# Optimization experiments

Measured on AMD Instinct MI355X. Metric: run time of the kernel, lower is better.

The kernel has to match this reference:

```python
import jax, jax.numpy as jnp
import numpy as np

C_IN = 2048
N_EXP = 64
TOPK = 2


def setup_inputs() -> dict:
    key = jax.random.key(0)
    kx, kw, kb = jax.random.split(key, 3)
    x = jax.random.normal(kx, (4, 4096, C_IN), dtype=jnp.float32)
    # nn.Linear(c_in, n_exp): weight [n_exp, c_in], bias [n_exp]
    bound = 1.0 / np.sqrt(C_IN)
    W = jax.random.uniform(kw, (N_EXP, C_IN), minval=-bound, maxval=bound, dtype=jnp.float32)
    b = jax.random.uniform(kb, (N_EXP,), minval=-bound, maxval=bound, dtype=jnp.float32)
    return {"x": x, "W": W, "b": b}


def reference(x, W, b):
    # linear: [B,S,C] @ [C,E] + [E] -> [B,S,E]
    logits = jnp.einsum("bsc,ec->bse", x, W) + b
    probs = jax.nn.softmax(logits, axis=-1)
    vals, idx = jax.lax.top_k(probs, TOPK)  # [B,S,K]
    # scatter top-k values back to full expert dim; other entries zero
    onehot = jax.nn.one_hot(idx, N_EXP, dtype=probs.dtype)  # [B,S,K,E]
    gate_out = jnp.einsum("bsk,bske->bse", vals, onehot)
    return gate_out
```

## Files before the change

### kernel.cpp

```cpp
#include <hip/hip_runtime.h>
#include <math.h>

#define C_IN 2048
#define N_EXP 64
#define TPB 16
#define KWIN 512
#define KSTEPS 16
#define DELTA  3e-4f
#define DELTA2 1e-3f

typedef __bf16 bf16x8 __attribute__((ext_vector_type(8)));
typedef float f32x4 __attribute__((ext_vector_type(4)));

__device__ __forceinline__ void cvt_split(float f, ushort& h, ushort& l) {
    uint u = __float_as_uint(f);
    uint hr = (u + (0x7FFFu + ((u >> 16) & 1u))) >> 16;
    h = (ushort)hr;
    float hf = __uint_as_float(hr << 16);
    uint v = __float_as_uint(f - hf);
    l = (ushort)((v + (0x7FFFu + ((v >> 16) & 1u))) >> 16);
}

__global__ void conv_w_kernel(const float* __restrict__ W,
                              ushort* __restrict__ whf, ushort* __restrict__ wlf) {
    const int o = blockIdx.x * 256 + threadIdx.x;
    const int egks = o >> 9;
    const int lane = (o >> 3) & 63;
    const int j = o & 7;
    const int e = (egks >> 6) * 16 + (lane & 15);
    const int k = (egks & 63) * 32 + (lane >> 4) * 8 + j;
    ushort h, lo;
    cvt_split(W[e * C_IN + k], h, lo);
    whf[o] = h;
    wlf[o] = lo;
}

__global__ __launch_bounds__(256, 4) void topk_gate_kernel(
    const float* __restrict__ x, const float* __restrict__ Wf,
    const float* __restrict__ b, const ushort* __restrict__ whf,
    const ushort* __restrict__ wlf, float* __restrict__ out)
{
    __shared__ float part[4][TPB][65];

    const int tid = threadIdx.x;
    const int wv = tid >> 6, l = tid & 63;
    const int t0 = blockIdx.x * TPB;
    const int tr = l & 15;
    const int kg = l >> 4;

    const float* xg = x + (size_t)(t0 + tr) * C_IN + wv * KWIN + kg * 8;

    f32x4 acc[4];
#pragma unroll
    for (int eg = 0; eg < 4; ++eg) acc[eg] = (f32x4){0.f, 0.f, 0.f, 0.f};

#pragma unroll 2
    for (int ks = 0; ks < KSTEPS; ++ks) {
        const float4 a0 = *(const float4*)(xg + ks * 32);
        const float4 a1 = *(const float4*)(xg + ks * 32 + 4);
        const int ksa = wv * KSTEPS + ks;
        uint4 wb[8];
#pragma unroll
        for (int eg = 0; eg < 4; ++eg) {
            wb[eg * 2 + 0] = *(const uint4*)&whf[(eg * 64 + ksa) * 512 + l * 8];
            wb[eg * 2 + 1] = *(const uint4*)&wlf[(eg * 64 + ksa) * 512 + l * 8];
        }
        ushort h[8], q[8];
        cvt_split(a0.x, h[0], q[0]); cvt_split(a0.y, h[1], q[1]);
        cvt_split(a0.z, h[2], q[2]); cvt_split(a0.w, h[3], q[3]);
        cvt_split(a1.x, h[4], q[4]); cvt_split(a1.y, h[5], q[5]);
        cvt_split(a1.z, h[6], q[6]); cvt_split(a1.w, h[7], q[7]);
        uint4 hv = {(uint)h[0] | ((uint)h[1] << 16), (uint)h[2] | ((uint)h[3] << 16),
                    (uint)h[4] | ((uint)h[5] << 16), (uint)h[6] | ((uint)h[7] << 16)};
        uint4 qv = {(uint)q[0] | ((uint)q[1] << 16), (uint)q[2] | ((uint)q[3] << 16),
                    (uint)q[4] | ((uint)q[5] << 16), (uint)q[6] | ((uint)q[7] << 16)};
        bf16x8 ah = __builtin_bit_cast(bf16x8, hv);
        bf16x8 al = __builtin_bit_cast(bf16x8, qv);
#pragma unroll
        for (int eg = 0; eg < 4; ++eg) {
            bf16x8 bh = __builtin_bit_cast(bf16x8, wb[eg * 2 + 0]);
            bf16x8 bl = __builtin_bit_cast(bf16x8, wb[eg * 2 + 1]);
            acc[eg] = __builtin_amdgcn_mfma_f32_16x16x32_bf16(ah, bh, acc[eg], 0, 0, 0);
            acc[eg] = __builtin_amdgcn_mfma_f32_16x16x32_bf16(al, bh, acc[eg], 0, 0, 0);
            acc[eg] = __builtin_amdgcn_mfma_f32_16x16x32_bf16(ah, bl, acc[eg], 0, 0, 0);
        }
    }

#pragma unroll
    for (int eg = 0; eg < 4; ++eg)
#pragma unroll
    for (int r = 0; r < 4; ++r)
        part[wv][kg * 4 + r][eg * 16 + tr] = acc[eg][r];
    __syncthreads();

    const int e = l;
    const float be = b[e];
    for (int ti = 0; ti < 4; ++ti) {
        const int t = wv * 4 + ti;
        float logit = part[0][t][e] + part[1][t][e]
                    + part[2][t][e] + part[3][t][e] + be;

        float v1, v2, v3; int i1, i2;
        for (int pass = 0; pass < 2; ++pass) {
            v1 = logit; i1 = e;
#pragma unroll
            for (int off = 32; off >= 1; off >>= 1) {
                float ov = __shfl_xor(v1, off, 64);
                int   oi = __shfl_xor(i1, off, 64);
                if (ov > v1 || (ov == v1 && oi < i1)) { v1 = ov; i1 = oi; }
            }
            v2 = (e == i1) ? -3.4e38f : logit;
            i2 = (e == i1) ? N_EXP : e;
#pragma unroll
            for (int off = 32; off >= 1; off >>= 1) {
                float ov = __shfl_xor(v2, off, 64);
                int   oi = __shfl_xor(i2, off, 64);
                if (ov > v2 || (ov == v2 && oi < i2)) { v2 = ov; i2 = oi; }
            }
            v3 = (e == i1 || e == i2) ? -3.4e38f : logit;
#pragma unroll
            for (int off = 32; off >= 1; off >>= 1) {
                float ov = __shfl_xor(v3, off, 64);
                v3 = (ov > v3) ? ov : v3;
            }
            if (pass == 1) break;
            const bool risky = (v1 - v2 < DELTA) || (v2 - v3 < DELTA);
            if (!risky) break;
            unsigned long long cm = __ballot(logit >= v2 - DELTA2);
            const float* xr = x + (size_t)(t0 + t) * C_IN;
            while (cm) {
                const int ce = __ffsll((unsigned long long)cm) - 1;
                cm &= cm - 1;
                const float* wr = Wf + (size_t)ce * C_IN;
                float p = 0.f;
#pragma unroll 8
                for (int i = 0; i < 32; ++i)
                    p = fmaf(xr[l + 64 * i], wr[l + 64 * i], p);
#pragma unroll
                for (int off = 32; off >= 1; off >>= 1)
                    p += __shfl_xor(p, off, 64);
                if (e == ce) logit = p + be;
            }
        }

        float ex = expf(logit - v1);
        float ssum = ex;
#pragma unroll
        for (int off = 32; off >= 1; off >>= 1)
            ssum += __shfl_xor(ssum, off, 64);
        const float inv = 1.0f / ssum;
        const float p1 = inv;
        const float p2 = expf(v2 - v1) * inv;
        const float o = (e == i1) ? p1 : ((e == i2) ? p2 : 0.0f);
        out[(size_t)(t0 + t) * N_EXP + e] = o;
    }
}

extern "C" void kernel_launch(void* const* d_in, const int* in_sizes, int n_in,
                              void* d_out, int out_size, void* d_ws, size_t ws_size,
                              hipStream_t stream) {
    const float* x = (const float*)d_in[0];
    const float* W = (const float*)d_in[1];
    const float* b = (const float*)d_in[2];
    float* out = (float*)d_out;

    ushort* whf = (ushort*)d_ws;
    ushort* wlf = whf + N_EXP * C_IN;

    conv_w_kernel<<<512, 256, 0, stream>>>(W, whf, wlf);

    const int tokens = in_sizes[0] / C_IN;
    const int grid = tokens / TPB;
    topk_gate_kernel<<<grid, 256, 0, stream>>>(x, W, b, whf, wlf, out);
}
```

Before: 56.47 us.

## Stage x and split weights through double-buffered LDS with async global-to-LDS loads

The kernel now handles 64 tokens per block, one 16-token group per wave, and steps through K in 16 slices. Each slice of x (with an XOR swizzle) and of the pre-split bf16 weights is loaded straight into double-buffered LDS using global_load_lds, with the next slice issued before the current one is computed. The weights are now shared across four times as many tokens per block and the cross-wave partial reduction is gone. In exchange, each block uses 128KB of LDS at one block per CU, which leaves fewer blocks to hide the full vmcnt waits and barriers taken every slice.

Result: slower. 83.78 us (+48.4%).

```diff
diff --git a/kernel.cpp b/kernel.cpp
--- a/kernel.cpp
+++ b/kernel.cpp
@@ -3,9 +3,8 @@
 
 #define C_IN 2048
 #define N_EXP 64
-#define TPB 16
-#define KWIN 512
-#define KSTEPS 16
+#define TPB 64
+#define NSLICE 16
 #define DELTA  3e-4f
 #define DELTA2 1e-3f
 
@@ -35,70 +34,108 @@
     wlf[o] = lo;
 }
 
-__global__ __launch_bounds__(256, 4) void topk_gate_kernel(
+__device__ __forceinline__ void glds16(const void* g, void* l) {
+    __builtin_amdgcn_global_load_lds(
+        (const __attribute__((address_space(1))) uint32_t*)g,
+        (__attribute__((address_space(3))) uint32_t*)l, 16, 0, 0);
+}
+
+__device__ __forceinline__ void cvt8(const float4 a, const float4 b2,
+                                     uint4& hv, uint4& lv) {
+    ushort h[8], q[8];
+    cvt_split(a.x, h[0], q[0]);  cvt_split(a.y, h[1], q[1]);
+    cvt_split(a.z, h[2], q[2]);  cvt_split(a.w, h[3], q[3]);
+    cvt_split(b2.x, h[4], q[4]); cvt_split(b2.y, h[5], q[5]);
+    cvt_split(b2.z, h[6], q[6]); cvt_split(b2.w, h[7], q[7]);
+    hv = (uint4){(uint)h[0] | ((uint)h[1] << 16), (uint)h[2] | ((uint)h[3] << 16),
+                 (uint)h[4] | ((uint)h[5] << 16), (uint)h[6] | ((uint)h[7] << 16)};
+    lv = (uint4){(uint)q[0] | ((uint)q[1] << 16), (uint)q[2] | ((uint)q[3] << 16),
+                 (uint)q[4] | ((uint)q[5] << 16), (uint)q[6] | ((uint)q[7] << 16)};
+}
+
+#define ISSUE(SC1) do {                                                       \
+    char* wdst_ = smem + 65536 + ((SC1) & 1) * 32768;                         \
+    _Pragma("unroll") for (int ks_ = 0; ks_ < 4; ++ks_) {                     \
+        const size_t so_ = ((size_t)(w * 64 + (SC1) * 4 + ks_)) * 512 + l * 8;\
+        glds16(whf + so_, wdst_ + (w * 4 + ks_) * 2048);                      \
+        glds16(wlf + so_, wdst_ + (w * 4 + ks_) * 2048 + 1024);               \
+    }                                                                         \
+    char* xdst_ = smem + ((SC1) & 1) * 32768;                                 \
+    _Pragma("unroll") for (int i_ = 0; i_ < 8; ++i_) {                        \
+        const int r_ = w * 16 + 2 * i_ + (l >> 5);                            \
+        const int sw_ = ((l & 31) * 16) ^ ((r_ & 15) << 5);                   \
+        glds16((const char*)x + (size_t)(t0 + r_) * 8192 + (SC1) * 512 + sw_, \
+               xdst_ + (w * 16 + 2 * i_) * 512);                              \
+    }                                                                         \
+    __builtin_amdgcn_sched_barrier(0);                                        \
+} while (0)
+
+__global__ __launch_bounds__(256, 1) void topk_gate_kernel(
     const float* __restrict__ x, const float* __restrict__ Wf,
     const float* __restrict__ b, const ushort* __restrict__ whf,
     const ushort* __restrict__ wlf, float* __restrict__ out)
 {
-    __shared__ float part[4][TPB][65];
+    __shared__ __align__(16) char smem[131072];
 
     const int tid = threadIdx.x;
-    const int wv = tid >> 6, l = tid & 63;
+    const int w = tid >> 6, l = tid & 63;
+    const int tr = l & 15, kq = l >> 4;
     const int t0 = blockIdx.x * TPB;
-    const int tr = l & 15;
-    const int kg = l >> 4;
-
-    const float* xg = x + (size_t)(t0 + tr) * C_IN + wv * KWIN + kg * 8;
 
     f32x4 acc[4];
 #pragma unroll
     for (int eg = 0; eg < 4; ++eg) acc[eg] = (f32x4){0.f, 0.f, 0.f, 0.f};
 
-#pragma unroll 2
-    for (int ks = 0; ks < KSTEPS; ++ks) {
-        const float4 a0 = *(const float4*)(xg + ks * 32);
-        const float4 a1 = *(const float4*)(xg + ks * 32 + 4);
-        const int ksa = wv * KSTEPS + ks;
-        uint4 wb[8];
-#pragma unroll
-        for (int eg = 0; eg < 4; ++eg) {
-            wb[eg * 2 + 0] = *(const uint4*)&whf[(eg * 64 + ksa) * 512 + l * 8];
-            wb[eg * 2 + 1] = *(const uint4*)&wlf[(eg * 64 + ksa) * 512 + l * 8];
-        }
-        ushort h[8], q[8];
-        cvt_split(a0.x, h[0], q[0]); cvt_split(a0.y, h[1], q[1]);
-        cvt_split(a0.z, h[2], q[2]); cvt_split(a0.w, h[3], q[3]);
-        cvt_split(a1.x, h[4], q[4]); cvt_split(a1.y, h[5], q[5]);
-        cvt_split(a1.z, h[6], q[6]); cvt_split(a1.w, h[7], q[7]);
-        uint4 hv = {(uint)h[0] | ((uint)h[1] << 16), (uint)h[2] | ((uint)h[3] << 16),
-                    (uint)h[4] | ((uint)h[5] << 16), (uint)h[6] | ((uint)h[7] << 16)};
-        uint4 qv = {(uint)q[0] | ((uint)q[1] << 16), (uint)q[2] | ((uint)q[3] << 16),
-                    (uint)q[4] | ((uint)q[5] << 16), (uint)q[6] | ((uint)q[7] << 16)};
-        bf16x8 ah = __builtin_bit_cast(bf16x8, hv);
-        bf16x8 al = __builtin_bit_cast(bf16x8, qv);
-#pragma unroll
-        for (int eg = 0; eg < 4; ++eg) {
-            bf16x8 bh = __builtin_bit_cast(bf16x8, wb[eg * 2 + 0]);
-            bf16x8 bl = __builtin_bit_cast(bf16x8, wb[eg * 2 + 1]);
-            acc[eg] = __builtin_amdgcn_mfma_f32_16x16x32_bf16(ah, bh, acc[eg], 0, 0, 0);
-            acc[eg] = __builtin_amdgcn_mfma_f32_16x16x32_bf16(al, bh, acc[eg], 0, 0, 0);
-            acc[eg] = __builtin_amdgcn_mfma_f32_16x16x32_bf16(ah, bl, acc[eg], 0, 0, 0);
+    ISSUE(0);
+
+#pragma unroll 1
+    for (int sc = 0; sc < NSLICE; ++sc) {
+        asm volatile("s_waitcnt vmcnt(0)" ::: "memory");
+        __builtin_amdgcn_sched_barrier(0);
+        asm volatile("s_waitcnt lgkmcnt(0)" ::: "memory");
+        __builtin_amdgcn_sched_barrier(0);
+        __builtin_amdgcn_s_barrier();
+        if (sc + 1 < NSLICE) ISSUE(sc + 1);
+
+        const char* xb = smem + (sc & 1) * 32768 + (w * 16) * 512;
+        const char* wb = smem + 65536 + (sc & 1) * 32768;
+#pragma unroll
+        for (int J = 0; J < 4; ++J) {
+            const int ao = tr * 512 + ((J * 128 + kq * 32) ^ (tr << 5));
+            float4 a0 = *(const float4*)(xb + ao);
+            float4 a1 = *(const float4*)(xb + ao + 16);
+            uint4 hv, lv;
+            cvt8(a0, a1, hv, lv);
+            bf16x8 ah = __builtin_bit_cast(bf16x8, hv);
+            bf16x8 al = __builtin_bit_cast(bf16x8, lv);
+            __builtin_amdgcn_s_setprio(1);
+#pragma unroll
+            for (int eg = 0; eg < 4; ++eg) {
+                uint4 bhu = *(const uint4*)(wb + (eg * 4 + J) * 2048 + l * 16);
+                uint4 blu = *(const uint4*)(wb + (eg * 4 + J) * 2048 + 1024 + l * 16);
+                bf16x8 bh = __builtin_bit_cast(bf16x8, bhu);
+                bf16x8 bl = __builtin_bit_cast(bf16x8, blu);
+                acc[eg] = __builtin_amdgcn_mfma_f32_16x16x32_bf16(ah, bh, acc[eg], 0, 0, 0);
+                acc[eg] = __builtin_amdgcn_mfma_f32_16x16x32_bf16(al, bh, acc[eg], 0, 0, 0);
+                acc[eg] = __builtin_amdgcn_mfma_f32_16x16x32_bf16(ah, bl, acc[eg], 0, 0, 0);
+            }
+            __builtin_amdgcn_s_setprio(0);
         }
     }
 
+    float* part = (float*)smem;
 #pragma unroll
     for (int eg = 0; eg < 4; ++eg)
 #pragma unroll
     for (int r = 0; r < 4; ++r)
-        part[wv][kg * 4 + r][eg * 16 + tr] = acc[eg][r];
+        part[(w * 16 + kq * 4 + r) * 65 + eg * 16 + tr] = acc[eg][r];
     __syncthreads();
 
     const int e = l;
     const float be = b[e];
-    for (int ti = 0; ti < 4; ++ti) {
-        const int t = wv * 4 + ti;
-        float logit = part[0][t][e] + part[1][t][e]
-                    + part[2][t][e] + part[3][t][e] + be;
+    for (int ti = 0; ti < 16; ++ti) {
+        const int t = w * 16 + ti;
+        float logit = part[t * 65 + e] + be;
 
         float v1, v2, v3; int i1, i2;
         for (int pass = 0; pass < 2; ++pass) {
```

## Stage x tiles in LDS via async global_load_lds with pipelined weight ring

Applied to the files above, without the earlier changes.

Restructures the gate GEMM so each block handles 64 tokens in four 16-token passes. Each pass stages the full x rows into swizzled shared memory with direct global-to-LDS loads, and streams weight fragments through a 3-slot per-wave ring with explicit vmcnt waits. Each wave now owns 16 experts over the full K range instead of a K-slice over all experts, which removes the cross-wave partial-sum reduction. The activation split into high and low bf16 parts now truncates instead of rounding. The 152KB of LDS limits occupancy to one block per CU, so the design relies on the software pipeline to hide latency.

Result: slower. 150.5 us (+166.5%).

```diff
diff --git a/kernel.cpp b/kernel.cpp
--- a/kernel.cpp
+++ b/kernel.cpp
@@ -3,22 +3,16 @@
 
 #define C_IN 2048
 #define N_EXP 64
-#define TPB 16
-#define KWIN 512
-#define KSTEPS 16
 #define DELTA  3e-4f
 #define DELTA2 1e-3f
 
 typedef __bf16 bf16x8 __attribute__((ext_vector_type(8)));
 typedef float f32x4 __attribute__((ext_vector_type(4)));
 
-__device__ __forceinline__ void cvt_split(float f, ushort& h, ushort& l) {
+__device__ __forceinline__ ushort bf16_rne(float f) {
     uint u = __float_as_uint(f);
-    uint hr = (u + (0x7FFFu + ((u >> 16) & 1u))) >> 16;
-    h = (ushort)hr;
-    float hf = __uint_as_float(hr << 16);
-    uint v = __float_as_uint(f - hf);
-    l = (ushort)((v + (0x7FFFu + ((v >> 16) & 1u))) >> 16);
+    u += 0x7FFFu + ((u >> 16) & 1u);
+    return (ushort)(u >> 16);
 }
 
 __global__ void conv_w_kernel(const float* __restrict__ W,
@@ -29,130 +23,185 @@
     const int j = o & 7;
     const int e = (egks >> 6) * 16 + (lane & 15);
     const int k = (egks & 63) * 32 + (lane >> 4) * 8 + j;
-    ushort h, lo;
-    cvt_split(W[e * C_IN + k], h, lo);
+    const float f = W[e * C_IN + k];
+    const ushort h = bf16_rne(f);
     whf[o] = h;
-    wlf[o] = lo;
-}
-
-__global__ __launch_bounds__(256, 4) void topk_gate_kernel(
+    wlf[o] = bf16_rne(f - __uint_as_float((uint)h << 16));
+}
+
+__device__ __forceinline__ void glds16(const void* g, void* l) {
+    __builtin_amdgcn_global_load_lds(
+        (const __attribute__((address_space(1))) uint32_t*)g,
+        (__attribute__((address_space(3))) uint32_t*)l, 16, 0, 0);
+}
+
+__device__ __forceinline__ void cvt8t(const float4 a, const float4 b,
+                                      uint4& hv, uint4& lv) {
+    const float fx[8] = {a.x, a.y, a.z, a.w, b.x, b.y, b.z, b.w};
+#pragma unroll
+    for (int p = 0; p < 4; ++p) {
+        const uint u0 = __float_as_uint(fx[2 * p]);
+        const uint u1 = __float_as_uint(fx[2 * p + 1]);
+        const float d0 = fx[2 * p] - __uint_as_float(u0 & 0xFFFF0000u);
+        const float d1 = fx[2 * p + 1] - __uint_as_float(u1 & 0xFFFF0000u);
+        hv[p] = (u0 >> 16) | (u1 & 0xFFFF0000u);
+        lv[p] = (__float_as_uint(d0) >> 16) | (__float_as_uint(d1) & 0xFFFF0000u);
+    }
+}
+
+#define WAIT4 do { asm volatile("s_waitcnt vmcnt(4)" ::: "memory");           \
+                   __builtin_amdgcn_sched_barrier(0); } while (0)
+#define WAIT0 do { asm volatile("s_waitcnt vmcnt(0)" ::: "memory");           \
+                   __builtin_amdgcn_sched_barrier(0); } while (0)
+
+#define WISS2(JV, WSLOT) do {                                                 \
+    glds16(whp + (size_t)((JV) + 2) * 512, wring + (WSLOT) * 2048 + l * 16);  \
+    glds16(wlp + (size_t)((JV) + 2) * 512, wring + (WSLOT) * 2048 + 1024 + l * 16); \
+    __builtin_amdgcn_sched_barrier(0);                                        \
+} while (0)
+
+#define KBODY(JV, SLOT) do {                                                  \
+    const int u_ = (JV) * 8 + kq * 2;                                         \
+    float4 a0 = *(const float4*)(smem + tr * 8192 + ((u_ ^ sw) * 16));        \
+    float4 a1 = *(const float4*)(smem + tr * 8192 + (((u_ + 1) ^ sw) * 16));  \
+    uint4 bhu = *(const uint4*)(wring + (SLOT) * 2048 + l * 16);              \
+    uint4 blu = *(const uint4*)(wring + (SLOT) * 2048 + 1024 + l * 16);       \
+    uint4 hv, lv;                                                             \
+    cvt8t(a0, a1, hv, lv);                                                    \
+    bf16x8 ah = __builtin_bit_cast(bf16x8, hv);                               \
+    bf16x8 al = __builtin_bit_cast(bf16x8, lv);                               \
+    bf16x8 bh = __builtin_bit_cast(bf16x8, bhu);                              \
+    bf16x8 bl = __builtin_bit_cast(bf16x8, blu);                              \
+    __builtin_amdgcn_s_setprio(1);                                            \
+    acc = __builtin_amdgcn_mfma_f32_16x16x32_bf16(ah, bh, acc, 0, 0, 0);      \
+    acc = __builtin_amdgcn_mfma_f32_16x16x32_bf16(al, bh, acc, 0, 0, 0);      \
+    acc = __builtin_amdgcn_mfma_f32_16x16x32_bf16(ah, bl, acc, 0, 0, 0);      \
+    __builtin_amdgcn_s_setprio(0);                                            \
+} while (0)
+
+#define KS(JV, SLOT, WSLOT) do { WISS2(JV, WSLOT); WAIT4; KBODY(JV, SLOT); } while (0)
+
+__global__ __launch_bounds__(256) void topk_gate_kernel(
     const float* __restrict__ x, const float* __restrict__ Wf,
     const float* __restrict__ b, const ushort* __restrict__ whf,
     const ushort* __restrict__ wlf, float* __restrict__ out)
 {
-    __shared__ float part[4][TPB][65];
+    __shared__ __align__(16) char smem[155648];
 
     const int tid = threadIdx.x;
-    const int wv = tid >> 6, l = tid & 63;
-    const int t0 = blockIdx.x * TPB;
-    const int tr = l & 15;
-    const int kg = l >> 4;
-
-    const float* xg = x + (size_t)(t0 + tr) * C_IN + wv * KWIN + kg * 8;
-
-    f32x4 acc[4];
-#pragma unroll
-    for (int eg = 0; eg < 4; ++eg) acc[eg] = (f32x4){0.f, 0.f, 0.f, 0.f};
-
-#pragma unroll 2
-    for (int ks = 0; ks < KSTEPS; ++ks) {
-        const float4 a0 = *(const float4*)(xg + ks * 32);
-        const float4 a1 = *(const float4*)(xg + ks * 32 + 4);
-        const int ksa = wv * KSTEPS + ks;
-        uint4 wb[8];
-#pragma unroll
-        for (int eg = 0; eg < 4; ++eg) {
-            wb[eg * 2 + 0] = *(const uint4*)&whf[(eg * 64 + ksa) * 512 + l * 8];
-            wb[eg * 2 + 1] = *(const uint4*)&wlf[(eg * 64 + ksa) * 512 + l * 8];
-        }
-        ushort h[8], q[8];
-        cvt_split(a0.x, h[0], q[0]); cvt_split(a0.y, h[1], q[1]);
-        cvt_split(a0.z, h[2], q[2]); cvt_split(a0.w, h[3], q[3]);
-        cvt_split(a1.x, h[4], q[4]); cvt_split(a1.y, h[5], q[5]);
-        cvt_split(a1.z, h[6], q[6]); cvt_split(a1.w, h[7], q[7]);
-        uint4 hv = {(uint)h[0] | ((uint)h[1] << 16), (uint)h[2] | ((uint)h[3] << 16),
-                    (uint)h[4] | ((uint)h[5] << 16), (uint)h[6] | ((uint)h[7] << 16)};
-        uint4 qv = {(uint)q[0] | ((uint)q[1] << 16), (uint)q[2] | ((uint)q[3] << 16),
-                    (uint)q[4] | ((uint)q[5] << 16), (uint)q[6] | ((uint)q[7] << 16)};
-        bf16x8 ah = __builtin_bit_cast(bf16x8, hv);
-        bf16x8 al = __builtin_bit_cast(bf16x8, qv);
-#pragma unroll
-        for (int eg = 0; eg < 4; ++eg) {
-            bf16x8 bh = __builtin_bit_cast(bf16x8, wb[eg * 2 + 0]);
-            bf16x8 bl = __builtin_bit_cast(bf16x8, wb[eg * 2 + 1]);
-            acc[eg] = __builtin_amdgcn_mfma_f32_16x16x32_bf16(ah, bh, acc[eg], 0, 0, 0);
-            acc[eg] = __builtin_amdgcn_mfma_f32_16x16x32_bf16(al, bh, acc[eg], 0, 0, 0);
-            acc[eg] = __builtin_amdgcn_mfma_f32_16x16x32_bf16(ah, bl, acc[eg], 0, 0, 0);
-        }
-    }
-
-#pragma unroll
-    for (int eg = 0; eg < 4; ++eg)
-#pragma unroll
-    for (int r = 0; r < 4; ++r)
-        part[wv][kg * 4 + r][eg * 16 + tr] = acc[eg][r];
-    __syncthreads();
-
-    const int e = l;
-    const float be = b[e];
-    for (int ti = 0; ti < 4; ++ti) {
-        const int t = wv * 4 + ti;
-        float logit = part[0][t][e] + part[1][t][e]
-                    + part[2][t][e] + part[3][t][e] + be;
-
-        float v1, v2, v3; int i1, i2;
-        for (int pass = 0; pass < 2; ++pass) {
-            v1 = logit; i1 = e;
-#pragma unroll
-            for (int off = 32; off >= 1; off >>= 1) {
-                float ov = __shfl_xor(v1, off, 64);
-                int   oi = __shfl_xor(i1, off, 64);
-                if (ov > v1 || (ov == v1 && oi < i1)) { v1 = ov; i1 = oi; }
+    const int w = tid >> 6, l = tid & 63;
+    const int tr = l & 15, kq = l >> 4;
+    const int sw = tr & 7;
+
+    const ushort* whp = whf + (size_t)(w * 64) * 512 + l * 8;
+    const ushort* wlp = wlf + (size_t)(w * 64) * 512 + l * 8;
+    char* wring = smem + 131072 + w * 6144;
+
+    const float be = b[l];
+
+#pragma unroll 1
+    for (int p = 0; p < 4; ++p) {
+        const int tokBaseP = blockIdx.x * 64 + p * 16;
+        const float* xgp = x + (size_t)tokBaseP * C_IN;
+
+        WISS2(-2, 0);
+        WISS2(-1, 1);
+
+#pragma unroll
+        for (int j2 = 0; j2 < 32; ++j2) {
+            const int r = j2 >> 1;
+            const int us = tid + (j2 & 1) * 256;
+            const size_t srcU = (size_t)r * 512 + (us ^ (r & 7));
+            glds16((const char*)xgp + srcU * 16, smem + j2 * 4096 + tid * 16);
+        }
+        __builtin_amdgcn_sched_barrier(0);
+        __syncthreads();
+
+        f32x4 acc = {0.f, 0.f, 0.f, 0.f};
+        {
+            WISS2(0, 2); KBODY(0, 0);
+            WISS2(1, 0); WAIT4; KBODY(1, 1);
+            WISS2(2, 1); WAIT4; KBODY(2, 2);
+        }
+#pragma unroll 1
+        for (int m = 0; m < 5; ++m) {
+            const int jb = 3 + 12 * m;
+            KS(jb + 0, 0, 2); KS(jb + 1, 1, 0); KS(jb + 2, 2, 1);
+            KS(jb + 3, 0, 2); KS(jb + 4, 1, 0); KS(jb + 5, 2, 1);
+            KS(jb + 6, 0, 2); KS(jb + 7, 1, 0); KS(jb + 8, 2, 1);
+            KS(jb + 9, 0, 2); KS(jb + 10, 1, 0); KS(jb + 11, 2, 1);
+        }
+        {
+            WAIT0; KBODY(63, 0);
+        }
+        __syncthreads();
+
+        float* part = (float*)smem;
+#pragma unroll
+        for (int r = 0; r < 4; ++r)
+            part[(kq * 4 + r) * 65 + w * 16 + tr] = acc[r];
+        __syncthreads();
+
+        const int e = l;
+        for (int ti = 0; ti < 4; ++ti) {
+            const int t = w * 4 + ti;
+            float logit = part[t * 65 + e] + be;
+
+            float v1, v2, v3; int i1, i2;
+            for (int pass = 0; pass < 2; ++pass) {
+                v1 = logit; i1 = e;
+#pragma unroll
+                for (int off = 32; off >= 1; off >>= 1) {
+                    float ov = __shfl_xor(v1, off, 64);
+                    int   oi = __shfl_xor(i1, off, 64);
+                    if (ov > v1 || (ov == v1 && oi < i1)) { v1 = ov; i1 = oi; }
+                }
+                v2 = (e == i1) ? -3.4e38f : logit;
+                i2 = (e == i1) ? N_EXP : e;
+#pragma unroll
+                for (int off = 32; off >= 1; off >>= 1) {
+                    float ov = __shfl_xor(v2, off, 64);
+                    int   oi = __shfl_xor(i2, off, 64);
+                    if (ov > v2 || (ov == v2 && oi < i2)) { v2 = ov; i2 = oi; }
+                }
+                v3 = (e == i1 || e == i2) ? -3.4e38f : logit;
+#pragma unroll
+                for (int off = 32; off >= 1; off >>= 1) {
+                    float ov = __shfl_xor(v3, off, 64);
+                    v3 = (ov > v3) ? ov : v3;
+                }
+                if (pass == 1) break;
+                const bool risky = (v1 - v2 < DELTA) || (v2 - v3 < DELTA);
+                if (!risky) break;
+                unsigned long long cm = __ballot(logit >= v2 - DELTA2);
+                const float* xr = x + (size_t)(tokBaseP + t) * C_IN;
+                while (cm) {
+                    const int ce = __ffsll((unsigned long long)cm) - 1;
+                    cm &= cm - 1;
+                    const float* wr = Wf + (size_t)ce * C_IN;
+                    float pr = 0.f;
+#pragma unroll 8
+                    for (int i = 0; i < 32; ++i)
+                        pr = fmaf(xr[l + 64 * i], wr[l + 64 * i], pr);
+#pragma unroll
+                    for (int off = 32; off >= 1; off >>= 1)
+                        pr += __shfl_xor(pr, off, 64);
+                    if (e == ce) logit = pr + be;
+                }
             }
-            v2 = (e == i1) ? -3.4e38f : logit;
-            i2 = (e == i1) ? N_EXP : e;
-#pragma unroll
-            for (int off = 32; off >= 1; off >>= 1) {
-                float ov = __shfl_xor(v2, off, 64);
-                int   oi = __shfl_xor(i2, off, 64);
-                if (ov > v2 || (ov == v2 && oi < i2)) { v2 = ov; i2 = oi; }
-            }
-            v3 = (e == i1 || e == i2) ? -3.4e38f : logit;
-#pragma unroll
-            for (int off = 32; off >= 1; off >>= 1) {
-                float ov = __shfl_xor(v3, off, 64);
-                v3 = (ov > v3) ? ov : v3;
-            }
-            if (pass == 1) break;
-            const bool risky = (v1 - v2 < DELTA) || (v2 - v3 < DELTA);
-            if (!risky) break;
-            unsigned long long cm = __ballot(logit >= v2 - DELTA2);
-            const float* xr = x + (size_t)(t0 + t) * C_IN;
-            while (cm) {
-                const int ce = __ffsll((unsigned long long)cm) - 1;
-                cm &= cm - 1;
-                const float* wr = Wf + (size_t)ce * C_IN;
-                float p = 0.f;
-#pragma unroll 8
-                for (int i = 0; i < 32; ++i)
-                    p = fmaf(xr[l + 64 * i], wr[l + 64 * i], p);
-#pragma unroll
-                for (int off = 32; off >= 1; off >>= 1)
-                    p += __shfl_xor(p, off, 64);
-                if (e == ce) logit = p + be;
-            }
-        }
-
-        float ex = expf(logit - v1);
-        float ssum = ex;
-#pragma unroll
-        for (int off = 32; off >= 1; off >>= 1)
-            ssum += __shfl_xor(ssum, off, 64);
-        const float inv = 1.0f / ssum;
-        const float p1 = inv;
-        const float p2 = expf(v2 - v1) * inv;
-        const float o = (e == i1) ? p1 : ((e == i2) ? p2 : 0.0f);
-        out[(size_t)(t0 + t) * N_EXP + e] = o;
+
+            float ex = expf(logit - v1);
+            float ssum = ex;
+#pragma unroll
+            for (int off = 32; off >= 1; off >>= 1)
+                ssum += __shfl_xor(ssum, off, 64);
+            const float inv = 1.0f / ssum;
+            const float p1 = inv;
+            const float p2 = expf(v2 - v1) * inv;
+            const float o = (e == i1) ? p1 : ((e == i2) ? p2 : 0.0f);
+            out[(size_t)(tokBaseP + t) * N_EXP + e] = o;
+        }
+        __syncthreads();
     }
 }
 
@@ -170,6 +219,6 @@
     conv_w_kernel<<<512, 256, 0, stream>>>(W, whf, wlf);
 
     const int tokens = in_sizes[0] / C_IN;
-    const int grid = tokens / TPB;
+    const int grid = tokens / 64;
     topk_gate_kernel<<<grid, 256, 0, stream>>>(x, W, b, whf, wlf, out);
 }
```
